# Kernel optimization log

Hardware: AMD Instinct MI355X
Metric: run time of the kernel (lower is better)

## Reference

```python
import jax, jax.numpy as jnp
import numpy as np
import math

B, L, D = 2, 2048, 1024
H, KV, HD = 16, 4, 64          # num_heads, num_kv_heads, head_dim
GROUPS = H // KV
ROPE_BASE = 10000.0


def _alibi_slopes(n_heads):
    def pow2(n):
        start = 2.0 ** (-(2.0 ** (-(math.log2(n) - 3))))
        return [start * (start ** i) for i in range(n)]
    if math.log2(n_heads).is_integer():
        return pow2(n_heads)
    c = 2 ** math.floor(math.log2(n_heads))
    return pow2(c) + _alibi_slopes(2 * c)[0::2][: n_heads - c]


def _rope_cos_sin(seq_len, dim, dtype):
    inv_freq = 1.0 / (ROPE_BASE ** (jnp.arange(0, dim, 2, dtype=jnp.float32) / dim))
    t = jnp.arange(seq_len, dtype=jnp.float32)
    freqs = t[:, None] * inv_freq[None, :]          # [L, dim/2]
    emb = jnp.concatenate([freqs, freqs], axis=-1)  # [L, dim]
    return jnp.cos(emb).astype(dtype), jnp.sin(emb).astype(dtype)


def _rotate_half(x):
    x1, x2 = x[..., : x.shape[-1] // 2], x[..., x.shape[-1] // 2 :]
    return jnp.concatenate([-x2, x1], axis=-1)


def setup_inputs() -> dict:
    key = jax.random.key(0)
    ks = jax.random.split(key, 5)
    s = 0.02
    return {
        "x": jax.random.normal(ks[0], (B, L, D), jnp.float32),
        "Wq": jax.random.normal(ks[1], (D, H * HD), jnp.float32) * s,
        "Wk": jax.random.normal(ks[2], (D, KV * HD), jnp.float32) * s,
        "Wv": jax.random.normal(ks[3], (D, KV * HD), jnp.float32) * s,
        "Wo": jax.random.normal(ks[4], (H * HD, D), jnp.float32) * s,
    }


def reference(x, Wq, Wk, Wv, Wo):
    b, l, _ = x.shape
    q = (x @ Wq).reshape(b, l, H, HD).transpose(0, 2, 1, 3)   # [B,H,L,hd]
    k = (x @ Wk).reshape(b, l, KV, HD).transpose(0, 2, 1, 3)  # [B,KV,L,hd]
    v = (x @ Wv).reshape(b, l, KV, HD).transpose(0, 2, 1, 3)
    # MQA broadcast: repeat_interleave over head dim
    k = jnp.repeat(k, GROUPS, axis=1)  # [B,H,L,hd]
    v = jnp.repeat(v, GROUPS, axis=1)

    cos, sin = _rope_cos_sin(l, HD, x.dtype)  # [L,hd]
    q = q * cos + _rotate_half(q) * sin
    k = k * cos + _rotate_half(k) * sin

    attn = jnp.einsum("bhqd,bhkd->bhqk", q, k) / math.sqrt(HD)
    # ALiBi bias: (j - i) * slope_h
    pos = jnp.arange(l)
    rel = (pos[None, :] - pos[:, None]).astype(x.dtype)        # [L,L]
    slopes = jnp.asarray(_alibi_slopes(H), dtype=x.dtype)      # [H]
    attn = attn + slopes[None, :, None, None] * rel[None, None, :, :]

    attn = jax.nn.softmax(attn, axis=-1)
    out = jnp.einsum("bhqk,bhkd->bhqd", attn, v)               # [B,H,L,hd]
    out = out.transpose(0, 2, 1, 3).reshape(b, l, H * HD)
    return out @ Wo
```

## Files before the change

kernel.cpp:

```cpp
#include <hip/hip_runtime.h>
#include <math.h>

typedef unsigned short u16;
typedef unsigned int u32;
typedef __attribute__((ext_vector_type(8))) short short8;
typedef __attribute__((ext_vector_type(4))) short short4v;
typedef __attribute__((ext_vector_type(4))) float floatx4;
typedef __attribute__((ext_vector_type(2))) unsigned int uint2v;

#define HN 16
#define KVN 4
#define HDN 64
#define BN_ 2
#define LN 2048
#define DN 1024

__device__ __forceinline__ u16 f2bf(float f) {
    u32 u = __float_as_uint(f);
    u32 r = (u + 0x7fffu + ((u >> 16) & 1u)) >> 16;
    return (u16)r;
}

__device__ __forceinline__ u32 pack2bf(float f0, float f1) {
    u32 u0 = __float_as_uint(f0);
    u32 u1 = __float_as_uint(f1);
    u0 += 0x7fffu + ((u0 >> 16) & 1u);
    u1 += 0x7fffu + ((u1 >> 16) & 1u);
    return __builtin_amdgcn_perm(u1, u0, 0x07060302u);
}

__device__ __forceinline__ void gl16(const u16* g, u16* l) {
    __builtin_amdgcn_global_load_lds(
        (const __attribute__((address_space(1))) u32*)g,
        (__attribute__((address_space(3))) u32*)l, 16, 0, 0);
}

__global__ __launch_bounds__(256) void cast_x_kernel(const float* __restrict__ x,
                                                     u16* __restrict__ xb, int n4) {
    int i = blockIdx.x * 256 + threadIdx.x;
    if (i < n4) {
        floatx4 v = ((const floatx4*)x)[i];
        short4v o;
        o[0] = (short)f2bf(v[0]);
        o[1] = (short)f2bf(v[1]);
        o[2] = (short)f2bf(v[2]);
        o[3] = (short)f2bf(v[3]);
        ((short4v*)xb)[i] = o;
    }
}

__global__ __launch_bounds__(256) void transpose_cast(const float* __restrict__ W,
                                                      u16* __restrict__ WT, int R, int C) {
    __shared__ float t[32][33];
    int tx = threadIdx.x & 31, ty = threadIdx.x >> 5;
    int c0 = blockIdx.x * 32, r0 = blockIdx.y * 32;
#pragma unroll
    for (int i = 0; i < 4; i++) {
        int r = r0 + ty + i * 8;
        t[ty + i * 8][tx] = W[(size_t)r * C + c0 + tx];
    }
    __syncthreads();
#pragma unroll
    for (int i = 0; i < 4; i++) {
        int c = c0 + ty + i * 8;
        WT[(size_t)c * R + r0 + tx] = f2bf(t[tx][ty + i * 8]);
    }
}

__global__ __launch_bounds__(256) void gemm_bf16_f32(const u16* __restrict__ A,
                                                     const u16* __restrict__ BT,
                                                     float* __restrict__ C,
                                                     int M, int N, int K) {
    __shared__ u16 sm[12288];
    int tid = threadIdx.x;
    int w = tid >> 6, l = tid & 63, quad = l >> 4, l16 = l & 15;
    int wm = (w >> 1) * 64, wn = (w & 1) * 32;
    floatx4 acc[4][2];
#pragma unroll
    for (int i = 0; i < 4; i++)
#pragma unroll
        for (int j = 0; j < 2; j++) acc[i][j] = (floatx4){0.f, 0.f, 0.f, 0.f};
    const u16* ag0 = A + (size_t)(blockIdx.y * 128 + 16 * w + (l >> 2)) * K + (l & 3) * 8;
    const u16* ag1 = ag0 + (size_t)64 * K;
    const u16* bg = BT + (size_t)(blockIdx.x * 64 + 16 * w + (l >> 2)) * K + (l & 3) * 8;
    int lbase = w * 512 + l * 8;
    gl16(ag0, &sm[lbase]);
    gl16(ag1, &sm[2048 + lbase]);
    gl16(bg, &sm[4096 + lbase]);
    int nit = K >> 5;
    for (int it = 0; it < nit; it++) {
        __syncthreads();
        int cur = it & 1;
        if (it + 1 < nit) {
            int nb = (cur ^ 1) * 6144;
            ag0 += 32; ag1 += 32; bg += 32;
            gl16(ag0, &sm[nb + lbase]);
            gl16(ag1, &sm[nb + 2048 + lbase]);
            gl16(bg, &sm[nb + 4096 + lbase]);
        }
        const u16* smc = &sm[cur * 6144];
        short8 af[4], bfr[2];
#pragma unroll
        for (int mt = 0; mt < 4; mt++) af[mt] = *(const short8*)&smc[(wm + mt * 16 + l16) * 32 + quad * 8];
#pragma unroll
        for (int nt = 0; nt < 2; nt++) bfr[nt] = *(const short8*)&smc[4096 + (wn + nt * 16 + l16) * 32 + quad * 8];
#pragma unroll
        for (int mt = 0; mt < 4; mt++)
#pragma unroll
            for (int nt = 0; nt < 2; nt++)
                acc[mt][nt] = __builtin_amdgcn_mfma_f32_16x16x32_bf16(af[mt], bfr[nt], acc[mt][nt], 0, 0, 0);
    }
#pragma unroll
    for (int mt = 0; mt < 4; mt++)
#pragma unroll
        for (int nt = 0; nt < 2; nt++)
#pragma unroll
            for (int r = 0; r < 4; r++) {
                int row = blockIdx.y * 128 + wm + mt * 16 + quad * 4 + r;
                int col = blockIdx.x * 64 + wn + nt * 16 + l16;
                C[(size_t)row * N + col] = acc[mt][nt][r];
            }
}

__global__ __launch_bounds__(256) void rope_scatter(const float* __restrict__ QKV,
                                                    u16* __restrict__ Qb,
                                                    u16* __restrict__ Kb,
                                                    u16* __restrict__ Vt) {
    int row = blockIdx.x;
    int b = row >> 11;
    int l = row & 2047;
    const float* src = QKV + (size_t)row * 1536;
    int t = threadIdx.x;
    const float LOG1E4_32 = 0.28782313662425572f;
    for (int p = t; p < 512; p += 256) {
        int hh = p >> 5, i = p & 31;
        float x1 = src[hh * 64 + i], x2 = src[hh * 64 + i + 32];
        float invf = expf(-(float)i * LOG1E4_32);
        float fr = (float)l * invf;
        float s, c;
        sincosf(fr, &s, &c);
        size_t base = (((size_t)b * HN + hh) * LN + l) * HDN;
        Qb[base + i] = f2bf(x1 * c - x2 * s);
        Qb[base + i + 32] = f2bf(x2 * c + x1 * s);
    }
    if (t < 128) {
        int kv = t >> 5, i = t & 31;
        float x1 = src[1024 + kv * 64 + i], x2 = src[1024 + kv * 64 + i + 32];
        float invf = expf(-(float)i * LOG1E4_32);
        float fr = (float)l * invf;
        float s, c;
        sincosf(fr, &s, &c);
        size_t base = (((size_t)b * KVN + kv) * LN + l) * HDN;
        Kb[base + i] = f2bf(x1 * c - x2 * s);
        Kb[base + i + 32] = f2bf(x2 * c + x1 * s);
    }
    {
        int kv = t >> 6, d = t & 63;
        float v = src[1280 + kv * 64 + d];
        Vt[(((size_t)b * KVN + kv) * HDN + d) * LN + l] = f2bf(v);
    }
}

__global__ __launch_bounds__(256) void attention_kernel(const u16* __restrict__ Qb,
                                                        const u16* __restrict__ Kb,
                                                        const u16* __restrict__ Vt,
                                                        u16* __restrict__ AO) {
    __shared__ u16 sm[20992];
    int qb = blockIdx.x, h = blockIdx.y, b = blockIdx.z;
    int kv = h >> 2;
    int tid = threadIdx.x, w = tid >> 6, l = tid & 63, quad = l >> 4, l16 = l & 15;
    const u16* Kbase = Kb + (((size_t)b * KVN + kv) * LN) * HDN;
    const u16* Vbase = Vt + (((size_t)b * KVN + kv) * HDN) * LN;
    short8 bq[2][2];
#pragma unroll
    for (int t = 0; t < 2; t++) {
        const u16* Qrow = Qb + (((size_t)b * HN + h) * LN + qb * 128 + t * 64 + w * 16 + l16) * HDN;
        bq[t][0] = *(const short8*)&Qrow[quad * 8];
        bq[t][1] = *(const short8*)&Qrow[32 + quad * 8];
    }
    const float LOG2E = 1.4426950408889634f;
    float slope = exp2f(-0.5f * (float)(h + 1));
    float sLE = slope * LOG2E;
    float c1 = 0.125f * LOG2E;
    float koff[4][4];
#pragma unroll
    for (int nt = 0; nt < 4; nt++)
#pragma unroll
        for (int r = 0; r < 4; r++)
            koff[nt][r] = sLE * (float)(nt * 16 + quad * 4 + r - (LN - 1)) - 12.0f * LOG2E;
    float kbrun = 0.0f;
    float kstep = 64.0f * sLE;
    floatx4 O[2][4], lacc[2];
#pragma unroll
    for (int t = 0; t < 2; t++) {
        lacc[t] = (floatx4){0.f, 0.f, 0.f, 0.f};
#pragma unroll
        for (int md = 0; md < 4; md++) O[t][md] = (floatx4){0.f, 0.f, 0.f, 0.f};
    }
    short8 ones;
#pragma unroll
    for (int i = 0; i < 8; i++) ones[i] = (short)0x3F80;
    u16* pb = &sm[16384 + w * 1152];
    int lbase = w * 512 + l * 8;
    const u16* kg = Kbase + (size_t)(16 * w + (l >> 2)) * 64 + (l & 3) * 8;
    const u16* vg = Vbase + (size_t)(16 * w + (l >> 2)) * 2048 + (l & 3) * 8;
    gl16(kg, &sm[lbase]);
    gl16(kg + 32, &sm[2048 + lbase]);
    gl16(vg, &sm[8192 + lbase]);
    gl16(vg + 32, &sm[8192 + 2048 + lbase]);
    for (int it = 0; it < 32; it++) {
        __syncthreads();
        int cur = it & 1;
        if (it + 1 < 32) {
            int nb = (cur ^ 1) * 4096;
            kg += 4096;
            vg += 64;
            gl16(kg, &sm[nb + lbase]);
            gl16(kg + 32, &sm[nb + 2048 + lbase]);
            gl16(vg, &sm[8192 + nb + lbase]);
            gl16(vg + 32, &sm[8192 + nb + 2048 + lbase]);
        }
        const u16* kc = &sm[cur * 4096];
        const u16* vc = &sm[8192 + cur * 4096];
        short8 ak0[4], ak1[4], av0[4], av1[4];
#pragma unroll
        for (int nt = 0; nt < 4; nt++) {
            ak0[nt] = *(const short8*)&kc[(nt * 16 + l16) * 32 + quad * 8];
            ak1[nt] = *(const short8*)&kc[2048 + (nt * 16 + l16) * 32 + quad * 8];
        }
#pragma unroll
        for (int md = 0; md < 4; md++) {
            av0[md] = *(const short8*)&vc[(md * 16 + l16) * 32 + quad * 8];
            av1[md] = *(const short8*)&vc[2048 + (md * 16 + l16) * 32 + quad * 8];
        }
        float koff2[4][4];
#pragma unroll
        for (int nt = 0; nt < 4; nt++)
#pragma unroll
            for (int r = 0; r < 4; r++) koff2[nt][r] = koff[nt][r] + kbrun;
        kbrun += kstep;
#pragma unroll
        for (int t = 0; t < 2; t++) {
            floatx4 S[4];
#pragma unroll
            for (int nt = 0; nt < 4; nt++) {
                floatx4 sa = (floatx4){0.f, 0.f, 0.f, 0.f};
                sa = __builtin_amdgcn_mfma_f32_16x16x32_bf16(ak0[nt], bq[t][0], sa, 0, 0, 0);
                sa = __builtin_amdgcn_mfma_f32_16x16x32_bf16(ak1[nt], bq[t][1], sa, 0, 0, 0);
                S[nt] = sa;
            }
#pragma unroll
            for (int nt = 0; nt < 4; nt++) {
                float p0 = __builtin_amdgcn_exp2f(S[nt][0] * c1 + koff2[nt][0]);
                float p1 = __builtin_amdgcn_exp2f(S[nt][1] * c1 + koff2[nt][1]);
                float p2 = __builtin_amdgcn_exp2f(S[nt][2] * c1 + koff2[nt][2]);
                float p3 = __builtin_amdgcn_exp2f(S[nt][3] * c1 + koff2[nt][3]);
                uint2v pk;
                pk[0] = pack2bf(p0, p1);
                pk[1] = pack2bf(p2, p3);
                *(uint2v*)&pb[l16 * 72 + nt * 16 + quad * 4] = pk;
            }
            short8 bp0 = *(const short8*)&pb[l16 * 72 + quad * 8];
            short8 bp1 = *(const short8*)&pb[l16 * 72 + 32 + quad * 8];
#pragma unroll
            for (int md = 0; md < 4; md++) {
                O[t][md] = __builtin_amdgcn_mfma_f32_16x16x32_bf16(av0[md], bp0, O[t][md], 0, 0, 0);
                O[t][md] = __builtin_amdgcn_mfma_f32_16x16x32_bf16(av1[md], bp1, O[t][md], 0, 0, 0);
            }
            lacc[t] = __builtin_amdgcn_mfma_f32_16x16x32_bf16(ones, bp0, lacc[t], 0, 0, 0);
            lacc[t] = __builtin_amdgcn_mfma_f32_16x16x32_bf16(ones, bp1, lacc[t], 0, 0, 0);
        }
    }
#pragma unroll
    for (int t = 0; t < 2; t++) {
        float inv = 1.0f / lacc[t][0];
        int qg = qb * 128 + t * 64 + w * 16 + l16;
        size_t base = ((size_t)b * LN + qg) * 1024 + h * 64 + quad * 4;
#pragma unroll
        for (int md = 0; md < 4; md++) {
            uint2v pk;
            pk[0] = pack2bf(O[t][md][0] * inv, O[t][md][1] * inv);
            pk[1] = pack2bf(O[t][md][2] * inv, O[t][md][3] * inv);
            *(uint2v*)&AO[base + md * 16] = pk;
        }
    }
}

extern "C" void kernel_launch(void* const* d_in, const int* in_sizes, int n_in,
                              void* d_out, int out_size, void* d_ws, size_t ws_size,
                              hipStream_t stream) {
    const float* x = (const float*)d_in[0];
    const float* Wq = (const float*)d_in[1];
    const float* Wk = (const float*)d_in[2];
    const float* Wv = (const float*)d_in[3];
    const float* Wo = (const float*)d_in[4];
    float* out = (float*)d_out;
    char* ws = (char*)d_ws;
    u16* xb = (u16*)(ws);
    u16* WT = (u16*)(ws + 8388608);
    u16* WoT = (u16*)(ws + 11534336);
    float* QKV = (float*)(ws + 13631488);
    u16* Qb = (u16*)(ws + 38797312);
    u16* Kb = (u16*)(ws + 47185920);
    u16* Vt = (u16*)(ws + 49283072);
    u16* AO = xb;

    cast_x_kernel<<<4096, 256, 0, stream>>>(x, xb, (BN_ * LN * DN) / 4);
    transpose_cast<<<dim3(1024 / 32, 1024 / 32), 256, 0, stream>>>(Wq, WT, 1024, 1024);
    transpose_cast<<<dim3(256 / 32, 1024 / 32), 256, 0, stream>>>(Wk, WT + 1024 * 1024, 1024, 256);
    transpose_cast<<<dim3(256 / 32, 1024 / 32), 256, 0, stream>>>(Wv, WT + 1280 * 1024, 1024, 256);
    transpose_cast<<<dim3(1024 / 32, 1024 / 32), 256, 0, stream>>>(Wo, WoT, 1024, 1024);
    gemm_bf16_f32<<<dim3(1536 / 64, 4096 / 128), 256, 0, stream>>>(xb, WT, QKV, 4096, 1536, 1024);
    rope_scatter<<<4096, 256, 0, stream>>>(QKV, Qb, Kb, Vt);
    attention_kernel<<<dim3(LN / 128, HN, BN_), 256, 0, stream>>>(Qb, Kb, Vt, AO);
    gemm_bf16_f32<<<dim3(1024 / 64, 4096 / 128), 256, 0, stream>>>(AO, WoT, out, 4096, 1024, 1024);
}
```

Baseline: 201.5 us.

## Skip ALiBi-negligible key blocks via persistent work queue with split-K atomics

Attention now runs as a persistent kernel. Blocks pull items from a global atomic counter and index a static table of per-head key-range chunks. The table keeps only the key spans where the ALiBi bias leaves non-negligible weight, so steep-slope heads process far fewer key blocks. Partial O and row sums are accumulated with float atomics into a zeroed buffer, and a new finalize kernel normalises them and casts to bf16. The change also adds a 128x128 GEMM tile for the QKV projection and uses fast intrinsic exp and sincos in RoPE. In exchange it adds a memset, atomic traffic and an extra launch, and it relies on scores staying bounded enough that the dropped keys are truly negligible.

Measured after the change: 302.4 us. +50.1%, slower.

```diff
diff --git a/kernel.cpp b/kernel.cpp
--- a/kernel.cpp
+++ b/kernel.cpp
@@ -65,6 +65,65 @@
         int c = c0 + ty + i * 8;
         WT[(size_t)c * R + r0 + tx] = f2bf(t[tx][ty + i * 8]);
     }
+}
+
+__global__ __launch_bounds__(256) void gemm128(const u16* __restrict__ A,
+                                               const u16* __restrict__ BT,
+                                               float* __restrict__ C,
+                                               int M, int N, int K) {
+    __shared__ u16 sm[16384];
+    int tid = threadIdx.x;
+    int w = tid >> 6, l = tid & 63, quad = l >> 4, l16 = l & 15;
+    int wm = (w >> 1) * 64, wn = (w & 1) * 64;
+    floatx4 acc[4][4];
+#pragma unroll
+    for (int i = 0; i < 4; i++)
+#pragma unroll
+        for (int j = 0; j < 4; j++) acc[i][j] = (floatx4){0.f, 0.f, 0.f, 0.f};
+    const u16* ag0 = A + (size_t)(blockIdx.y * 128 + (tid >> 2)) * K + (tid & 3) * 8;
+    const u16* ag1 = ag0 + (size_t)64 * K;
+    const u16* bg0 = BT + (size_t)(blockIdx.x * 128 + (tid >> 2)) * K + (tid & 3) * 8;
+    const u16* bg1 = bg0 + (size_t)64 * K;
+    int lbase = tid * 8;
+    gl16(ag0, &sm[lbase]);
+    gl16(ag1, &sm[2048 + lbase]);
+    gl16(bg0, &sm[4096 + lbase]);
+    gl16(bg1, &sm[6144 + lbase]);
+    int nit = K >> 5;
+    for (int it = 0; it < nit; it++) {
+        __syncthreads();
+        int cur = it & 1;
+        if (it + 1 < nit) {
+            int nb = (cur ^ 1) * 8192;
+            ag0 += 32; ag1 += 32; bg0 += 32; bg1 += 32;
+            gl16(ag0, &sm[nb + lbase]);
+            gl16(ag1, &sm[nb + 2048 + lbase]);
+            gl16(bg0, &sm[nb + 4096 + lbase]);
+            gl16(bg1, &sm[nb + 6144 + lbase]);
+        }
+        const u16* sa = &sm[cur * 8192];
+        const u16* sb = sa + 4096;
+        short8 af[4], bfr[4];
+#pragma unroll
+        for (int mt = 0; mt < 4; mt++) af[mt] = *(const short8*)&sa[(wm + mt * 16 + l16) * 32 + quad * 8];
+#pragma unroll
+        for (int nt = 0; nt < 4; nt++) bfr[nt] = *(const short8*)&sb[(wn + nt * 16 + l16) * 32 + quad * 8];
+#pragma unroll
+        for (int mt = 0; mt < 4; mt++)
+#pragma unroll
+            for (int nt = 0; nt < 4; nt++)
+                acc[mt][nt] = __builtin_amdgcn_mfma_f32_16x16x32_bf16(af[mt], bfr[nt], acc[mt][nt], 0, 0, 0);
+    }
+#pragma unroll
+    for (int mt = 0; mt < 4; mt++)
+#pragma unroll
+        for (int nt = 0; nt < 4; nt++)
+#pragma unroll
+            for (int r = 0; r < 4; r++) {
+                int row = blockIdx.y * 128 + wm + mt * 16 + quad * 4 + r;
+                int col = blockIdx.x * 128 + wn + nt * 16 + l16;
+                C[(size_t)row * N + col] = acc[mt][nt][r];
+            }
 }
 
 __global__ __launch_bounds__(256) void gemm_bf16_f32(const u16* __restrict__ A,
@@ -135,10 +194,10 @@
     for (int p = t; p < 512; p += 256) {
         int hh = p >> 5, i = p & 31;
         float x1 = src[hh * 64 + i], x2 = src[hh * 64 + i + 32];
-        float invf = expf(-(float)i * LOG1E4_32);
+        float invf = __expf(-(float)i * LOG1E4_32);
         float fr = (float)l * invf;
         float s, c;
-        sincosf(fr, &s, &c);
+        __sincosf(fr, &s, &c);
         size_t base = (((size_t)b * HN + hh) * LN + l) * HDN;
         Qb[base + i] = f2bf(x1 * c - x2 * s);
         Qb[base + i + 32] = f2bf(x2 * c + x1 * s);
@@ -146,10 +205,10 @@
     if (t < 128) {
         int kv = t >> 5, i = t & 31;
         float x1 = src[1024 + kv * 64 + i], x2 = src[1024 + kv * 64 + i + 32];
-        float invf = expf(-(float)i * LOG1E4_32);
+        float invf = __expf(-(float)i * LOG1E4_32);
         float fr = (float)l * invf;
         float s, c;
-        sincosf(fr, &s, &c);
+        __sincosf(fr, &s, &c);
         size_t base = (((size_t)b * KVN + kv) * LN + l) * HDN;
         Kb[base + i] = f2bf(x1 * c - x2 * s);
         Kb[base + i + 32] = f2bf(x2 * c + x1 * s);
@@ -161,129 +220,168 @@
     }
 }
 
+#define IT(h, ks, n) ((u32)(h) | ((u32)(ks) << 8) | ((u32)(n) << 24))
+#define NITEMS (37 * 32)
+static __device__ const u32 g_items[37] = {
+    IT(10, 512, 8),  IT(10, 1024, 8), IT(10, 1536, 8),
+    IT(11, 0, 8),    IT(11, 512, 8),  IT(11, 1024, 8), IT(11, 1536, 8),
+    IT(12, 0, 8),    IT(12, 512, 8),  IT(12, 1024, 8), IT(12, 1536, 8),
+    IT(13, 0, 8),    IT(13, 512, 8),  IT(13, 1024, 8), IT(13, 1536, 8),
+    IT(14, 0, 8),    IT(14, 512, 8),  IT(14, 1024, 8), IT(14, 1536, 8),
+    IT(15, 0, 8),    IT(15, 512, 8),  IT(15, 1024, 8), IT(15, 1536, 8),
+    IT(6, 1664, 6),  IT(8, 1280, 6),  IT(8, 1664, 6),  IT(9, 960, 6),  IT(9, 1344, 6),
+    IT(5, 1728, 5),  IT(7, 1472, 5),  IT(9, 1728, 5),
+    IT(7, 1792, 4),
+    IT(3, 1856, 3),  IT(4, 1856, 3),
+    IT(1, 1920, 2),  IT(2, 1920, 2),
+    IT(0, 1984, 1)};
+
 __global__ __launch_bounds__(256) void attention_kernel(const u16* __restrict__ Qb,
                                                         const u16* __restrict__ Kb,
                                                         const u16* __restrict__ Vt,
-                                                        u16* __restrict__ AO) {
+                                                        float* __restrict__ Oacc,
+                                                        float* __restrict__ lsumg,
+                                                        int* __restrict__ counter) {
     __shared__ u16 sm[20992];
-    int qb = blockIdx.x, h = blockIdx.y, b = blockIdx.z;
-    int kv = h >> 2;
+    __shared__ int s_item;
     int tid = threadIdx.x, w = tid >> 6, l = tid & 63, quad = l >> 4, l16 = l & 15;
-    const u16* Kbase = Kb + (((size_t)b * KVN + kv) * LN) * HDN;
-    const u16* Vbase = Vt + (((size_t)b * KVN + kv) * HDN) * LN;
-    short8 bq[2][2];
-#pragma unroll
-    for (int t = 0; t < 2; t++) {
-        const u16* Qrow = Qb + (((size_t)b * HN + h) * LN + qb * 128 + t * 64 + w * 16 + l16) * HDN;
-        bq[t][0] = *(const short8*)&Qrow[quad * 8];
-        bq[t][1] = *(const short8*)&Qrow[32 + quad * 8];
-    }
     const float LOG2E = 1.4426950408889634f;
-    float slope = exp2f(-0.5f * (float)(h + 1));
-    float sLE = slope * LOG2E;
-    float c1 = 0.125f * LOG2E;
-    float koff[4][4];
-#pragma unroll
-    for (int nt = 0; nt < 4; nt++)
-#pragma unroll
-        for (int r = 0; r < 4; r++)
-            koff[nt][r] = sLE * (float)(nt * 16 + quad * 4 + r - (LN - 1)) - 12.0f * LOG2E;
-    float kbrun = 0.0f;
-    float kstep = 64.0f * sLE;
-    floatx4 O[2][4], lacc[2];
-#pragma unroll
-    for (int t = 0; t < 2; t++) {
-        lacc[t] = (floatx4){0.f, 0.f, 0.f, 0.f};
-#pragma unroll
-        for (int md = 0; md < 4; md++) O[t][md] = (floatx4){0.f, 0.f, 0.f, 0.f};
-    }
-    short8 ones;
-#pragma unroll
-    for (int i = 0; i < 8; i++) ones[i] = (short)0x3F80;
     u16* pb = &sm[16384 + w * 1152];
     int lbase = w * 512 + l * 8;
-    const u16* kg = Kbase + (size_t)(16 * w + (l >> 2)) * 64 + (l & 3) * 8;
-    const u16* vg = Vbase + (size_t)(16 * w + (l >> 2)) * 2048 + (l & 3) * 8;
-    gl16(kg, &sm[lbase]);
-    gl16(kg + 32, &sm[2048 + lbase]);
-    gl16(vg, &sm[8192 + lbase]);
-    gl16(vg + 32, &sm[8192 + 2048 + lbase]);
-    for (int it = 0; it < 32; it++) {
+    for (;;) {
+        if (tid == 0) s_item = atomicAdd(counter, 1);
         __syncthreads();
-        int cur = it & 1;
-        if (it + 1 < 32) {
-            int nb = (cur ^ 1) * 4096;
-            kg += 4096;
-            vg += 64;
-            gl16(kg, &sm[nb + lbase]);
-            gl16(kg + 32, &sm[nb + 2048 + lbase]);
-            gl16(vg, &sm[8192 + nb + lbase]);
-            gl16(vg + 32, &sm[8192 + nb + 2048 + lbase]);
-        }
-        const u16* kc = &sm[cur * 4096];
-        const u16* vc = &sm[8192 + cur * 4096];
-        short8 ak0[4], ak1[4], av0[4], av1[4];
-#pragma unroll
-        for (int nt = 0; nt < 4; nt++) {
-            ak0[nt] = *(const short8*)&kc[(nt * 16 + l16) * 32 + quad * 8];
-            ak1[nt] = *(const short8*)&kc[2048 + (nt * 16 + l16) * 32 + quad * 8];
-        }
-#pragma unroll
-        for (int md = 0; md < 4; md++) {
-            av0[md] = *(const short8*)&vc[(md * 16 + l16) * 32 + quad * 8];
-            av1[md] = *(const short8*)&vc[2048 + (md * 16 + l16) * 32 + quad * 8];
-        }
-        float koff2[4][4];
+        int i = s_item;
+        if (i >= NITEMS) break;
+        u32 v = g_items[i >> 5];
+        int h = (int)(v & 255u), ks = (int)((v >> 8) & 0xFFFFu), nit = (int)(v >> 24);
+        int sub = i & 31, b = sub >> 4, qb = sub & 15;
+        int kv = h >> 2;
+        const u16* Kbase = Kb + (((size_t)b * KVN + kv) * LN) * HDN;
+        const u16* Vbase = Vt + (((size_t)b * KVN + kv) * HDN) * LN;
+        short8 bq[2][2];
+#pragma unroll
+        for (int t = 0; t < 2; t++) {
+            const u16* Qrow = Qb + (((size_t)b * HN + h) * LN + qb * 128 + t * 64 + w * 16 + l16) * HDN;
+            bq[t][0] = *(const short8*)&Qrow[quad * 8];
+            bq[t][1] = *(const short8*)&Qrow[32 + quad * 8];
+        }
+        float sLE = exp2f(-0.5f * (float)(h + 1)) * LOG2E;
+        float c1 = 0.125f * LOG2E;
+        float koff[4][4];
 #pragma unroll
         for (int nt = 0; nt < 4; nt++)
 #pragma unroll
-            for (int r = 0; r < 4; r++) koff2[nt][r] = koff[nt][r] + kbrun;
-        kbrun += kstep;
+            for (int r = 0; r < 4; r++)
+                koff[nt][r] = fmaf(sLE, (float)(ks + nt * 16 + quad * 4 + r - (LN - 1)), -17.312340491f);
+        float kbrun = 0.0f, kstep = 64.0f * sLE;
+        floatx4 O[2][4], lacc[2];
 #pragma unroll
         for (int t = 0; t < 2; t++) {
-            floatx4 S[4];
+            lacc[t] = (floatx4){0.f, 0.f, 0.f, 0.f};
+#pragma unroll
+            for (int md = 0; md < 4; md++) O[t][md] = (floatx4){0.f, 0.f, 0.f, 0.f};
+        }
+        short8 ones;
+#pragma unroll
+        for (int z = 0; z < 8; z++) ones[z] = (short)0x3F80;
+        const u16* kg = Kbase + (size_t)(ks + 16 * w + (l >> 2)) * 64 + (l & 3) * 8;
+        const u16* vg = Vbase + (size_t)(16 * w + (l >> 2)) * 2048 + ks + (l & 3) * 8;
+        gl16(kg, &sm[lbase]);
+        gl16(kg + 32, &sm[2048 + lbase]);
+        gl16(vg, &sm[8192 + lbase]);
+        gl16(vg + 32, &sm[8192 + 2048 + lbase]);
+        for (int it = 0; it < nit; it++) {
+            __syncthreads();
+            int cur = it & 1;
+            if (it + 1 < nit) {
+                int nb = (cur ^ 1) * 4096;
+                kg += 4096;
+                vg += 64;
+                gl16(kg, &sm[nb + lbase]);
+                gl16(kg + 32, &sm[nb + 2048 + lbase]);
+                gl16(vg, &sm[8192 + nb + lbase]);
+                gl16(vg + 32, &sm[8192 + nb + 2048 + lbase]);
+            }
+            const u16* kc = &sm[cur * 4096];
+            const u16* vc = &sm[8192 + cur * 4096];
+            short8 ak0[4], ak1[4], av0[4], av1[4];
 #pragma unroll
             for (int nt = 0; nt < 4; nt++) {
-                floatx4 sa = (floatx4){0.f, 0.f, 0.f, 0.f};
-                sa = __builtin_amdgcn_mfma_f32_16x16x32_bf16(ak0[nt], bq[t][0], sa, 0, 0, 0);
-                sa = __builtin_amdgcn_mfma_f32_16x16x32_bf16(ak1[nt], bq[t][1], sa, 0, 0, 0);
-                S[nt] = sa;
-            }
-#pragma unroll
-            for (int nt = 0; nt < 4; nt++) {
-                float p0 = __builtin_amdgcn_exp2f(S[nt][0] * c1 + koff2[nt][0]);
-                float p1 = __builtin_amdgcn_exp2f(S[nt][1] * c1 + koff2[nt][1]);
-                float p2 = __builtin_amdgcn_exp2f(S[nt][2] * c1 + koff2[nt][2]);
-                float p3 = __builtin_amdgcn_exp2f(S[nt][3] * c1 + koff2[nt][3]);
-                uint2v pk;
-                pk[0] = pack2bf(p0, p1);
-                pk[1] = pack2bf(p2, p3);
-                *(uint2v*)&pb[l16 * 72 + nt * 16 + quad * 4] = pk;
-            }
-            short8 bp0 = *(const short8*)&pb[l16 * 72 + quad * 8];
-            short8 bp1 = *(const short8*)&pb[l16 * 72 + 32 + quad * 8];
+                ak0[nt] = *(const short8*)&kc[(nt * 16 + l16) * 32 + quad * 8];
+                ak1[nt] = *(const short8*)&kc[2048 + (nt * 16 + l16) * 32 + quad * 8];
+            }
 #pragma unroll
             for (int md = 0; md < 4; md++) {
-                O[t][md] = __builtin_amdgcn_mfma_f32_16x16x32_bf16(av0[md], bp0, O[t][md], 0, 0, 0);
-                O[t][md] = __builtin_amdgcn_mfma_f32_16x16x32_bf16(av1[md], bp1, O[t][md], 0, 0, 0);
-            }
-            lacc[t] = __builtin_amdgcn_mfma_f32_16x16x32_bf16(ones, bp0, lacc[t], 0, 0, 0);
-            lacc[t] = __builtin_amdgcn_mfma_f32_16x16x32_bf16(ones, bp1, lacc[t], 0, 0, 0);
-        }
-    }
-#pragma unroll
-    for (int t = 0; t < 2; t++) {
-        float inv = 1.0f / lacc[t][0];
-        int qg = qb * 128 + t * 64 + w * 16 + l16;
-        size_t base = ((size_t)b * LN + qg) * 1024 + h * 64 + quad * 4;
-#pragma unroll
-        for (int md = 0; md < 4; md++) {
-            uint2v pk;
-            pk[0] = pack2bf(O[t][md][0] * inv, O[t][md][1] * inv);
-            pk[1] = pack2bf(O[t][md][2] * inv, O[t][md][3] * inv);
-            *(uint2v*)&AO[base + md * 16] = pk;
-        }
-    }
+                av0[md] = *(const short8*)&vc[(md * 16 + l16) * 32 + quad * 8];
+                av1[md] = *(const short8*)&vc[2048 + (md * 16 + l16) * 32 + quad * 8];
+            }
+            float koff2[4][4];
+#pragma unroll
+            for (int nt = 0; nt < 4; nt++)
+#pragma unroll
+                for (int r = 0; r < 4; r++) koff2[nt][r] = koff[nt][r] + kbrun;
+            kbrun += kstep;
+#pragma unroll
+            for (int t = 0; t < 2; t++) {
+                floatx4 S[4];
+#pragma unroll
+                for (int nt = 0; nt < 4; nt++) {
+                    floatx4 sa = (floatx4){0.f, 0.f, 0.f, 0.f};
+                    sa = __builtin_amdgcn_mfma_f32_16x16x32_bf16(ak0[nt], bq[t][0], sa, 0, 0, 0);
+                    sa = __builtin_amdgcn_mfma_f32_16x16x32_bf16(ak1[nt], bq[t][1], sa, 0, 0, 0);
+                    S[nt] = sa;
+                }
+#pragma unroll
+                for (int nt = 0; nt < 4; nt++) {
+                    float p0 = __builtin_amdgcn_exp2f(S[nt][0] * c1 + koff2[nt][0]);
+                    float p1 = __builtin_amdgcn_exp2f(S[nt][1] * c1 + koff2[nt][1]);
+                    float p2 = __builtin_amdgcn_exp2f(S[nt][2] * c1 + koff2[nt][2]);
+                    float p3 = __builtin_amdgcn_exp2f(S[nt][3] * c1 + koff2[nt][3]);
+                    uint2v pk;
+                    pk[0] = pack2bf(p0, p1);
+                    pk[1] = pack2bf(p2, p3);
+                    *(uint2v*)&pb[l16 * 72 + nt * 16 + quad * 4] = pk;
+                }
+                short8 bp0 = *(const short8*)&pb[l16 * 72 + quad * 8];
+                short8 bp1 = *(const short8*)&pb[l16 * 72 + 32 + quad * 8];
+#pragma unroll
+                for (int md = 0; md < 4; md++) {
+                    O[t][md] = __builtin_amdgcn_mfma_f32_16x16x32_bf16(av0[md], bp0, O[t][md], 0, 0, 0);
+                    O[t][md] = __builtin_amdgcn_mfma_f32_16x16x32_bf16(av1[md], bp1, O[t][md], 0, 0, 0);
+                }
+                lacc[t] = __builtin_amdgcn_mfma_f32_16x16x32_bf16(ones, bp0, lacc[t], 0, 0, 0);
+                lacc[t] = __builtin_amdgcn_mfma_f32_16x16x32_bf16(ones, bp1, lacc[t], 0, 0, 0);
+            }
+        }
+#pragma unroll
+        for (int t = 0; t < 2; t++) {
+            int q = qb * 128 + t * 64 + w * 16 + l16;
+            size_t base = (((size_t)b * HN + h) * LN + q) * 64;
+#pragma unroll
+            for (int md = 0; md < 4; md++)
+#pragma unroll
+                for (int r = 0; r < 4; r++)
+                    atomicAdd(&Oacc[base + md * 16 + quad * 4 + r], O[t][md][r]);
+            if (quad == 0) atomicAdd(&lsumg[((size_t)b * HN + h) * LN + q], lacc[t][0]);
+        }
+    }
+}
+
+__global__ __launch_bounds__(256) void finalize_kernel(const float* __restrict__ Oacc,
+                                                       const float* __restrict__ lsumg,
+                                                       u16* __restrict__ AO) {
+    int row = blockIdx.x;
+    int b = row >> 11, q = row & 2047;
+    int t = threadIdx.x;
+    int h = t >> 4, d4 = (t & 15) * 4;
+    size_t idx = ((size_t)b * HN + h) * LN + q;
+    floatx4 o = *(const floatx4*)&Oacc[idx * 64 + d4];
+    float inv = 1.0f / lsumg[idx];
+    uint2v pk;
+    pk[0] = pack2bf(o[0] * inv, o[1] * inv);
+    pk[1] = pack2bf(o[2] * inv, o[3] * inv);
+    *(uint2v*)&AO[(size_t)row * 1024 + h * 64 + d4] = pk;
 }
 
 extern "C" void kernel_launch(void* const* d_in, const int* in_sizes, int n_in,
@@ -304,14 +402,19 @@
     u16* Kb = (u16*)(ws + 47185920);
     u16* Vt = (u16*)(ws + 49283072);
     u16* AO = xb;
+    float* Oacc = (float*)(ws + 13631488);
+    float* lsumg = (float*)(ws + 30408704);
+    int* counter = (int*)(ws + 30670848);
 
     cast_x_kernel<<<4096, 256, 0, stream>>>(x, xb, (BN_ * LN * DN) / 4);
     transpose_cast<<<dim3(1024 / 32, 1024 / 32), 256, 0, stream>>>(Wq, WT, 1024, 1024);
     transpose_cast<<<dim3(256 / 32, 1024 / 32), 256, 0, stream>>>(Wk, WT + 1024 * 1024, 1024, 256);
     transpose_cast<<<dim3(256 / 32, 1024 / 32), 256, 0, stream>>>(Wv, WT + 1280 * 1024, 1024, 256);
     transpose_cast<<<dim3(1024 / 32, 1024 / 32), 256, 0, stream>>>(Wo, WoT, 1024, 1024);
-    gemm_bf16_f32<<<dim3(1536 / 64, 4096 / 128), 256, 0, stream>>>(xb, WT, QKV, 4096, 1536, 1024);
+    gemm128<<<dim3(1536 / 128, 4096 / 128), 256, 0, stream>>>(xb, WT, QKV, 4096, 1536, 1024);
     rope_scatter<<<4096, 256, 0, stream>>>(QKV, Qb, Kb, Vt);
-    attention_kernel<<<dim3(LN / 128, HN, BN_), 256, 0, stream>>>(Qb, Kb, Vt, AO);
+    hipMemsetAsync(ws + 13631488, 0, 17039616, stream);
+    attention_kernel<<<768, 256, 0, stream>>>(Qb, Kb, Vt, Oacc, lsumg, counter);
+    finalize_kernel<<<4096, 256, 0, stream>>>(Oacc, lsumg, AO);
     gemm_bf16_f32<<<dim3(1024 / 64, 4096 / 128), 256, 0, stream>>>(AO, WoT, out, 4096, 1024, 1024);
 }
```
